# Kernel tuning notes

Measured on AMD Instinct MI355X. Metric: run time of the kernel, lower is better.

The kernel has to match this reference:

```python
import jax, jax.numpy as jnp
import numpy as np

N = 50000      # n_nodes
E = 800000     # n_edges
IN_CH = 128
HID = 128
OUT_CH = 64
N_LAYERS = 4


def _linear_params(key, fan_in, fan_out):
    kw, kb = jax.random.split(key)
    bound = 1.0 / np.sqrt(fan_in)
    W = jax.random.uniform(kw, (fan_out, fan_in), jnp.float32, -bound, bound)
    b = jax.random.uniform(kb, (fan_out,), jnp.float32, -bound, bound)
    return W, b


def setup_inputs() -> dict:
    key = jax.random.key(0)
    ks = jax.random.split(key, 5)
    x = jax.random.normal(ks[0], (N, IN_CH), jnp.float32)
    edge_index = jax.random.randint(ks[1], (2, E), 0, N, dtype=jnp.int64)
    W_in, b_in = _linear_params(ks[2], IN_CH, HID)
    conv_keys = jax.random.split(ks[3], N_LAYERS)
    Wc = jnp.stack([_linear_params(k, HID, HID)[0] for k in conv_keys])
    bc = jnp.stack([_linear_params(k, HID, HID)[1] for k in conv_keys])
    W_out, b_out = _linear_params(ks[4], HID * N_LAYERS, OUT_CH)
    return {"x": x, "edge_index": edge_index, "W_in": W_in, "b_in": b_in,
            "Wc": Wc, "bc": bc, "W_out": W_out, "b_out": b_out}


def reference(x, edge_index, W_in, b_in, Wc, bc, W_out, b_out):
    n = x.shape[0]
    # input projection + relu
    x = jax.nn.relu(x @ W_in.T + b_in)
    src, dst = edge_index[0], edge_index[1]
    loop = jnp.arange(n, dtype=edge_index.dtype)
    src_a = jnp.concatenate([src, loop])   # [E+N]
    dst_a = jnp.concatenate([dst, loop])   # [E+N]
    # symmetric-normalized degree (with self loops)
    deg = jax.ops.segment_sum(jnp.ones(src_a.shape[0], x.dtype), dst_a, num_segments=n)
    norm = (deg[src_a] * deg[dst_a]) ** -0.5
    norm = jnp.where(jnp.isinf(norm), 0.0, norm)  # guard deg==0 (original sets inf->0)
    layer_outputs = []
    for i in range(Wc.shape[0]):
        h = x @ Wc[i].T + bc[i]                     # [N, HID]
        msg = h[src_a] * norm[:, None]              # gather + scale  [E+N, HID]
        out = jax.ops.segment_sum(msg, dst_a, num_segments=n)  # scatter-add
        x = jax.nn.relu(out)
        layer_outputs.append(x)
    h = jnp.concatenate(layer_outputs, axis=-1)     # jk_mode='cat' -> [N, HID*L]
    return h @ W_out.T + b_out
```

## Files before the change

kernel.cpp:

```cpp
#include <hip/hip_runtime.h>
#include <hip/hip_bf16.h>

#ifndef MIN
#define MIN(a,b) ((a)<(b)?(a):(b))
#endif

typedef _Float16 half2_t __attribute__((ext_vector_type(2)));
typedef _Float16 half4_t __attribute__((ext_vector_type(4)));
typedef _Float16 half8_t __attribute__((ext_vector_type(8)));
typedef float floatx4 __attribute__((ext_vector_type(4)));

#define BUCKET_SHIFT 6
#define BUCKET_SIZE 64
#define SCHUNK 2048


template <int KCH, bool A_F16, bool RELU, bool BIAS, bool SCALE, bool F16OUT>
__device__ __forceinline__
void gemm_body64(int rb, int ch, const void* __restrict__ Av, int lda,
                 const _Float16* __restrict__ W, int ldw,
                 const float* __restrict__ bias, const float* __restrict__ dinv,
                 void* __restrict__ Cv, int ldc, int M) {
    __shared__ __align__(16) _Float16 Ws[64][136];

    int tid = threadIdx.x;
    int rowBase = rb * 64;
    int colBase = ch * 64;
    int w = tid >> 6;
    int lane = tid & 63;
    int lrow = lane & 15;
    int quad = lane >> 4;
    int kq = quad * 8;
    int gr = rowBase + w * 16 + lrow;

    floatx4 acc[4];
#pragma unroll
    for (int nt = 0; nt < 4; ++nt) acc[nt] = (floatx4){0.f, 0.f, 0.f, 0.f};

#pragma unroll
    for (int kc = 0; kc < KCH; ++kc) {
#pragma unroll
        for (int i = tid; i < 64 * 16; i += 256) {
            int n = i >> 4, k8 = (i & 15) * 8;
            uint4 v = *(const uint4*)(W + (size_t)(colBase + n) * ldw + kc * 128 + k8);
            *(uint4*)(&Ws[n][k8]) = v;
        }
        __syncthreads();

        half8_t a[4];
        if (gr < M) {
            if (A_F16) {
                const _Float16* A = (const _Float16*)Av;
                const _Float16* ap = A + (size_t)gr * lda + kc * 128 + kq;
#pragma unroll
                for (int ks = 0; ks < 4; ++ks)
                    a[ks] = *(const half8_t*)(ap + ks * 32);
            } else {
                const float* A = (const float*)Av;
                const float* ap = A + (size_t)gr * lda + kc * 128 + kq;
#pragma unroll
                for (int ks = 0; ks < 4; ++ks) {
                    float4 v0 = *(const float4*)(ap + ks * 32);
                    float4 v1 = *(const float4*)(ap + ks * 32 + 4);
                    half8_t h;
                    h[0] = (_Float16)v0.x; h[1] = (_Float16)v0.y;
                    h[2] = (_Float16)v0.z; h[3] = (_Float16)v0.w;
                    h[4] = (_Float16)v1.x; h[5] = (_Float16)v1.y;
                    h[6] = (_Float16)v1.z; h[7] = (_Float16)v1.w;
                    a[ks] = h;
                }
            }
        } else {
#pragma unroll
            for (int ks = 0; ks < 4; ++ks)
                a[ks] = (half8_t){0, 0, 0, 0, 0, 0, 0, 0};
        }

#pragma unroll
        for (int ks = 0; ks < 4; ++ks) {
            int kk = ks * 32 + kq;
#pragma unroll
            for (int nt = 0; nt < 4; ++nt) {
                half8_t b = *(const half8_t*)(&Ws[nt * 16 + lrow][kk]);
                acc[nt] = __builtin_amdgcn_mfma_f32_16x16x32_f16(a[ks], b, acc[nt], 0, 0, 0);
            }
        }
        if (kc != KCH - 1) __syncthreads();
    }

#pragma unroll
    for (int nt = 0; nt < 4; ++nt) {
        int col = colBase + nt * 16 + lrow;
        float bv = BIAS ? bias[col] : 0.0f;
#pragma unroll
        for (int reg = 0; reg < 4; ++reg) {
            int gr2 = rowBase + w * 16 + quad * 4 + reg;
            if (gr2 < M) {
                float v = acc[nt][reg] + bv;
                if (RELU) v = fmaxf(v, 0.0f);
                if (SCALE) v *= dinv[gr2];
                if (F16OUT) {
                    _Float16* C = (_Float16*)Cv;
                    C[(size_t)gr2 * ldc + col] = (_Float16)v;
                } else {
                    float* C = (float*)Cv;
                    C[(size_t)gr2 * ldc + col] = v;
                }
            }
        }
    }
}

template <int KCH, bool A_F16, bool RELU, bool BIAS, bool SCALE, bool F16OUT, bool SPLIT>
__global__ __launch_bounds__(256)
void mfma_gemm64(const void* __restrict__ Av, int lda,
                 const _Float16* __restrict__ W, int ldw,
                 const float* __restrict__ bias, const float* __restrict__ dinv,
                 void* __restrict__ Cv, int ldc, int M) {
    int rb, ch;
    if (SPLIT) { rb = blockIdx.x >> 1; ch = blockIdx.x & 1; }
    else       { rb = blockIdx.x;      ch = 0; }
    gemm_body64<KCH, A_F16, RELU, BIAS, SCALE, F16OUT>(
        rb, ch, Av, lda, W, ldw, bias, dinv, Cv, ldc, M);
}


__global__ __launch_bounds__(256)
void k_hist_cvt(const int* __restrict__ dst, int E, int* __restrict__ bucketCnt, int NB,
                const float* __restrict__ a, _Float16* __restrict__ oa, int na,
                const float* __restrict__ b, _Float16* __restrict__ ob, int nb,
                const float* __restrict__ c, _Float16* __restrict__ oc, int nc,
                _Float16* __restrict__ zrow) {
    __shared__ int h[1024];
    int t = threadIdx.x;
    if (blockIdx.x < 512) {
        for (int i = t; i < 1024; i += 256) h[i] = 0;
        __syncthreads();
        for (int e = blockIdx.x * 256 + t; e < E; e += 512 * 256)
            atomicAdd(&h[dst[e] >> BUCKET_SHIFT], 1);
        __syncthreads();
        for (int i = t; i < NB; i += 256)
            if (h[i]) atomicAdd(&bucketCnt[i], h[i]);
    } else {
        int i = (blockIdx.x - 512) * 256 + t;
        if (i < na) oa[i] = (_Float16)a[i];
        if (i < nb) ob[i] = (_Float16)b[i];
        if (i < nc) oc[i] = (_Float16)c[i];
        if (i < 128) zrow[i] = (_Float16)0.0f;
    }
}

__global__ void bucket_scan(const int* __restrict__ bucketCnt,
                            int* __restrict__ bucketBase, int* __restrict__ bucketCur,
                            int NB, int E) {
    __shared__ int sm[1024];
    int t = threadIdx.x;
    int v = (t < NB) ? bucketCnt[t] : 0;
    sm[t] = v;
    __syncthreads();
    for (int off = 1; off < 1024; off <<= 1) {
        int add = (t >= off) ? sm[t - off] : 0;
        __syncthreads();
        sm[t] += add;
        __syncthreads();
    }
    if (t < NB) {
        bucketBase[t] = sm[t] - v;
        bucketCur[t] = sm[t] - v;
    }
    if (t == 0) bucketBase[NB] = E;
}


__global__ __launch_bounds__(256)
void k_scatter_proj(const int* __restrict__ src, const int* __restrict__ dst, int E,
                    int* __restrict__ bucketCur, unsigned int* __restrict__ rec, int SB,
                    const float* __restrict__ A, const _Float16* __restrict__ W,
                    const float* __restrict__ bias, _Float16* __restrict__ Cout, int M) {
    __shared__ int hist[1024];
    __shared__ int base[1024];
    if (blockIdx.x < SB) {
        int t = threadIdx.x;
        int e0 = blockIdx.x * SCHUNK;
        int e1 = MIN(E, e0 + SCHUNK);
        for (int i = t; i < 1024; i += 256) hist[i] = 0;
        __syncthreads();
        for (int e = e0 + t; e < e1; e += 256)
            atomicAdd(&hist[dst[e] >> BUCKET_SHIFT], 1);
        __syncthreads();
        for (int i = t; i < 1024; i += 256) {
            int c = hist[i];
            base[i] = c ? atomicAdd(&bucketCur[i], c) : 0;
            hist[i] = 0;
        }
        __syncthreads();
        for (int e = e0 + t; e < e1; e += 256) {
            int d = dst[e];
            int bk = d >> BUCKET_SHIFT;
            int pos = base[bk] + atomicAdd(&hist[bk], 1);
            rec[pos] = (unsigned)src[e] | ((unsigned)(d & (BUCKET_SIZE - 1)) << 16);
        }
    } else {
        int b2 = blockIdx.x - SB;
        gemm_body64<1, false, true, true, false, true>(
            b2 >> 1, b2 & 1, A, 128, W, 128, bias, nullptr, Cout, 128, M);
    }
}

__global__ void bucket_build(const unsigned int* __restrict__ rec,
                             const int* __restrict__ bucketBase,
                             int* __restrict__ rowptr, unsigned short* __restrict__ csr_src,
                             float* __restrict__ dinv, int N, int E) {
    __shared__ int lcnt[256];
    __shared__ int sm[256];
    __shared__ int lcur[64];
    int b = blockIdx.x;
    int t = threadIdx.x;
    int beg = bucketBase[b], end = bucketBase[b + 1];
    lcnt[t] = 0;
    __syncthreads();
    for (int i = beg + t; i < end; i += 256)
        atomicAdd(&lcnt[rec[i] >> 16], 1);
    __syncthreads();
    int v = lcnt[t];
    sm[t] = v;
    __syncthreads();
    for (int off = 1; off < 256; off <<= 1) {
        int add = (t >= off) ? sm[t - off] : 0;
        __syncthreads();
        sm[t] += add;
        __syncthreads();
    }
    int excl = sm[t] - v;
    if (t < BUCKET_SIZE) {
        int node = b * BUCKET_SIZE + t;
        if (node < N) {
            rowptr[node] = beg + excl;
            dinv[node] = rsqrtf((float)(v + 1));
        }
        lcur[t] = beg + excl;
    }
    __syncthreads();
    for (int i = beg + t; i < end; i += 256) {
        unsigned int r = rec[i];
        int pos = atomicAdd(&lcur[r >> 16], 1);
        csr_src[pos] = (unsigned short)(r & 0xFFFFu);
    }
    if (b == 0 && t == 0) rowptr[N] = E;
}


__global__ __launch_bounds__(256)
void agg_kernel(const half2_t* __restrict__ Hb, const float* __restrict__ dinv,
                const int* __restrict__ rowptr,
                const unsigned short* __restrict__ csr_src,
                half2_t* __restrict__ X, int N) {
    int node = blockIdx.x * 4 + (threadIdx.x >> 6);
    int t = threadIdx.x & 63;
    if (node >= N) return;
    float di = dinv[node];
    half2_t hu = Hb[(size_t)node * 64 + t];
    float2 acc;
    acc.x = (float)hu.x;
    acc.y = (float)hu.y;
    int beg = rowptr[node];
    int end = rowptr[node + 1];

    for (int base = beg; base < end; base += 64) {
        int idx = base + t;
        int s_lane = (idx < end) ? (int)csr_src[idx] : N;
        int m = end - base;
        if (m > 64) m = 64;
        int mm = (m + 15) & ~15;
        for (int j = 0; j < mm; j += 16) {
            int s[16];
#pragma unroll
            for (int k = 0; k < 16; ++k) s[k] = __shfl(s_lane, j + k);
            half2_t u[16];
#pragma unroll
            for (int k = 0; k < 16; ++k) u[k] = Hb[(size_t)s[k] * 64 + t];
#pragma unroll
            for (int k = 0; k < 16; ++k) {
                acc.x += (float)u[k].x;
                acc.y += (float)u[k].y;
            }
        }
    }
    half2_t o;
    o.x = (_Float16)fmaxf(acc.x * di, 0.0f);
    o.y = (_Float16)fmaxf(acc.y * di, 0.0f);
    X[(size_t)node * 256 + t] = o;
}


extern "C" void kernel_launch(void* const* d_in, const int* in_sizes, int n_in,
                              void* d_out, int out_size, void* d_ws, size_t ws_size,
                              hipStream_t stream) {
    const float* x     = (const float*)d_in[0];
    const int*   ei    = (const int*)d_in[1];
    const float* W_in  = (const float*)d_in[2];
    const float* b_in  = (const float*)d_in[3];
    const float* Wc    = (const float*)d_in[4];
    const float* bc    = (const float*)d_in[5];
    const float* W_out = (const float*)d_in[6];
    const float* b_out = (const float*)d_in[7];
    float* out = (float*)d_out;

    const int HID = 128;
    const int N = in_sizes[0] / HID;
    const int E = in_sizes[1] / 2;
    const int L = 4;
    const int* src = ei;
    const int* dst = ei + E;
    const int NB = (N + BUCKET_SIZE - 1) >> BUCKET_SHIFT;

    char* ws = (char*)d_ws;
    size_t off = 0;
    auto carve = [&](size_t bytes) {
        void* p = ws + off;
        off += (bytes + 255) & ~(size_t)255;
        return p;
    };
    float* dinv        = (float*)carve((size_t)N * 4);
    int*   rowptr      = (int*)carve((size_t)(N + 1) * 4);
    unsigned short* csr_src = (unsigned short*)carve((size_t)E * 2);
    unsigned int* rec  = (unsigned int*)carve((size_t)E * 4);
    int*   bucketCnt   = (int*)carve((size_t)1024 * 4);
    int*   bucketBase  = (int*)carve((size_t)1025 * 4);
    int*   bucketCur   = (int*)carve((size_t)1024 * 4);
    _Float16* bufA     = (_Float16*)carve((size_t)N * HID * 2);
    _Float16* bufH     = (_Float16*)carve((size_t)(N + 1) * HID * 2);
    _Float16* bufXcat  = (_Float16*)carve((size_t)N * 512 * 2);
    _Float16* Wf_in    = (_Float16*)carve((size_t)HID * HID * 2);
    _Float16* Wf_c     = (_Float16*)carve((size_t)L * HID * HID * 2);
    _Float16* Wf_out   = (_Float16*)carve((size_t)64 * 512 * 2);
    (void)ws_size;

    int gemm_blocks = (N + 63) / 64;
    int SB = (E + SCHUNK - 1) / SCHUNK;

    hipMemsetAsync(bucketCnt, 0, (size_t)1024 * 4, stream);
    k_hist_cvt<<<512 + 256, 256, 0, stream>>>(
        dst, E, bucketCnt, NB,
        W_in, Wf_in, HID * HID,
        Wc, Wf_c, L * HID * HID,
        W_out, Wf_out, 64 * 512,
        bufH + (size_t)N * HID);
    bucket_scan<<<1, 1024, 0, stream>>>(bucketCnt, bucketBase, bucketCur, NB, E);
    k_scatter_proj<<<SB + 2 * gemm_blocks, 256, 0, stream>>>(
        src, dst, E, bucketCur, rec, SB,
        x, Wf_in, b_in, bufA, N);
    bucket_build<<<NB, 256, 0, stream>>>(rec, bucketBase, rowptr, csr_src, dinv, N, E);

    for (int l = 0; l < L; ++l) {
        const void* Ain = (l == 0) ? (const void*)bufA
                                   : (const void*)(bufXcat + (size_t)(l - 1) * 128);
        int lda = (l == 0) ? 128 : 512;
        mfma_gemm64<1, true, false, true, true, true, true>
            <<<2 * gemm_blocks, 256, 0, stream>>>(Ain, lda, Wf_c + (size_t)l * HID * HID,
                                                  HID, bc + (size_t)l * HID, dinv,
                                                  bufH, HID, N);
        agg_kernel<<<(N + 3) / 4, 256, 0, stream>>>((const half2_t*)bufH, dinv, rowptr,
                                                    csr_src,
                                                    (half2_t*)bufXcat + (size_t)l * 64, N);
    }

    mfma_gemm64<4, true, false, true, false, false, false>
        <<<gemm_blocks, 256, 0, stream>>>(bufXcat, 512, Wf_out, 512, b_out, nullptr,
                                          out, 64, N);
}
```

Baseline: 310.3 us.

## Split hidden features into 32-column planes for cache-local aggregation passes

The conv GEMM now writes its fp16 output as four column planes of 32 features (each plane holds N+1 rows), not as row-major 128-wide rows. The aggregation kernel runs four passes, one per plane. In each pass a wavefront's 64 lanes gather four neighbors at once, 16 lanes per neighbor and 64 bytes each, and then reduce the partial sums with cross-lane shuffles. The goal is a smaller working set per pass (about 3.2 MB per plane) so random gathers stay in cache. The cost is four times as many agg blocks, shorter 64-byte gather segments, extra shuffle reductions, and scattered GEMM stores.

```diff
diff --git a/kernel.cpp b/kernel.cpp
--- a/kernel.cpp
+++ b/kernel.cpp
@@ -15,7 +15,7 @@
 #define SCHUNK 2048
 
 
-template <int KCH, bool A_F16, bool RELU, bool BIAS, bool SCALE, bool F16OUT>
+template <int KCH, bool A_F16, bool RELU, bool BIAS, bool SCALE, bool F16OUT, bool PLANES>
 __device__ __forceinline__
 void gemm_body64(int rb, int ch, const void* __restrict__ Av, int lda,
                  const _Float16* __restrict__ W, int ldw,
@@ -99,7 +99,11 @@
                 float v = acc[nt][reg] + bv;
                 if (RELU) v = fmaxf(v, 0.0f);
                 if (SCALE) v *= dinv[gr2];
-                if (F16OUT) {
+                if (PLANES) {
+                    _Float16* C = (_Float16*)Cv;
+                    int p = col >> 5, cc = col & 31;
+                    C[((size_t)p * (M + 1) + gr2) * 32 + cc] = (_Float16)v;
+                } else if (F16OUT) {
                     _Float16* C = (_Float16*)Cv;
                     C[(size_t)gr2 * ldc + col] = (_Float16)v;
                 } else {
@@ -111,7 +115,8 @@
     }
 }
 
-template <int KCH, bool A_F16, bool RELU, bool BIAS, bool SCALE, bool F16OUT, bool SPLIT>
+template <int KCH, bool A_F16, bool RELU, bool BIAS, bool SCALE, bool F16OUT, bool PLANES,
+          bool SPLIT>
 __global__ __launch_bounds__(256)
 void mfma_gemm64(const void* __restrict__ Av, int lda,
                  const _Float16* __restrict__ W, int ldw,
@@ -120,7 +125,7 @@
     int rb, ch;
     if (SPLIT) { rb = blockIdx.x >> 1; ch = blockIdx.x & 1; }
     else       { rb = blockIdx.x;      ch = 0; }
-    gemm_body64<KCH, A_F16, RELU, BIAS, SCALE, F16OUT>(
+    gemm_body64<KCH, A_F16, RELU, BIAS, SCALE, F16OUT, PLANES>(
         rb, ch, Av, lda, W, ldw, bias, dinv, Cv, ldc, M);
 }
 
@@ -130,7 +135,7 @@
                 const float* __restrict__ a, _Float16* __restrict__ oa, int na,
                 const float* __restrict__ b, _Float16* __restrict__ ob, int nb,
                 const float* __restrict__ c, _Float16* __restrict__ oc, int nc,
-                _Float16* __restrict__ zrow) {
+                _Float16* __restrict__ planes, int N) {
     __shared__ int h[1024];
     int t = threadIdx.x;
     if (blockIdx.x < 512) {
@@ -146,7 +151,10 @@
         if (i < na) oa[i] = (_Float16)a[i];
         if (i < nb) ob[i] = (_Float16)b[i];
         if (i < nc) oc[i] = (_Float16)c[i];
-        if (i < 128) zrow[i] = (_Float16)0.0f;
+        if (i < 128) {
+            int p = i >> 5, cc = i & 31;
+            planes[((size_t)p * (N + 1) + N) * 32 + cc] = (_Float16)0.0f;
+        }
     }
 }
 
@@ -202,7 +210,7 @@
         }
     } else {
         int b2 = blockIdx.x - SB;
-        gemm_body64<1, false, true, true, false, true>(
+        gemm_body64<1, false, true, true, false, true, false>(
             b2 >> 1, b2 & 1, A, 128, W, 128, bias, nullptr, Cout, 128, M);
     }
 }
@@ -251,20 +259,27 @@
 
 
 __global__ __launch_bounds__(256)
-void agg_kernel(const half2_t* __restrict__ Hb, const float* __restrict__ dinv,
+void agg_kernel(const half2_t* __restrict__ Hp, const float* __restrict__ dinv,
                 const int* __restrict__ rowptr,
                 const unsigned short* __restrict__ csr_src,
-                half2_t* __restrict__ X, int N) {
-    int node = blockIdx.x * 4 + (threadIdx.x >> 6);
+                half2_t* __restrict__ X, int N, int NBLK) {
+    int pass = blockIdx.x / NBLK;
+    int nb = blockIdx.x - pass * NBLK;
+    int node = nb * 4 + (threadIdx.x >> 6);
     int t = threadIdx.x & 63;
     if (node >= N) return;
+    int g = t >> 4;
+    int c = t & 15;
+    const half2_t* P = Hp + (size_t)pass * (N + 1) * 16;
     float di = dinv[node];
-    half2_t hu = Hb[(size_t)node * 64 + t];
+    int beg = rowptr[node];
+    int end = rowptr[node + 1];
+
+    int selfs = (g == 0) ? node : N;
+    half2_t hu = P[(size_t)selfs * 16 + c];
     float2 acc;
     acc.x = (float)hu.x;
     acc.y = (float)hu.y;
-    int beg = rowptr[node];
-    int end = rowptr[node + 1];
 
     for (int base = beg; base < end; base += 64) {
         int idx = base + t;
@@ -273,23 +288,32 @@
         if (m > 64) m = 64;
         int mm = (m + 15) & ~15;
         for (int j = 0; j < mm; j += 16) {
-            int s[16];
-#pragma unroll
-            for (int k = 0; k < 16; ++k) s[k] = __shfl(s_lane, j + k);
-            half2_t u[16];
-#pragma unroll
-            for (int k = 0; k < 16; ++k) u[k] = Hb[(size_t)s[k] * 64 + t];
-#pragma unroll
-            for (int k = 0; k < 16; ++k) {
-                acc.x += (float)u[k].x;
-                acc.y += (float)u[k].y;
-            }
-        }
-    }
-    half2_t o;
-    o.x = (_Float16)fmaxf(acc.x * di, 0.0f);
-    o.y = (_Float16)fmaxf(acc.y * di, 0.0f);
-    X[(size_t)node * 256 + t] = o;
+            int s0 = __shfl(s_lane, j + g);
+            int s1 = __shfl(s_lane, j + 4 + g);
+            int s2 = __shfl(s_lane, j + 8 + g);
+            int s3 = __shfl(s_lane, j + 12 + g);
+            half2_t u0 = P[(size_t)s0 * 16 + c];
+            half2_t u1 = P[(size_t)s1 * 16 + c];
+            half2_t u2 = P[(size_t)s2 * 16 + c];
+            half2_t u3 = P[(size_t)s3 * 16 + c];
+            acc.x += (float)u0.x; acc.y += (float)u0.y;
+            acc.x += (float)u1.x; acc.y += (float)u1.y;
+            acc.x += (float)u2.x; acc.y += (float)u2.y;
+            acc.x += (float)u3.x; acc.y += (float)u3.y;
+        }
+    }
+
+    acc.x += __shfl_xor(acc.x, 16);
+    acc.x += __shfl_xor(acc.x, 32);
+    acc.y += __shfl_xor(acc.y, 16);
+    acc.y += __shfl_xor(acc.y, 32);
+
+    if (g == 0) {
+        half2_t o;
+        o.x = (_Float16)fmaxf(acc.x * di, 0.0f);
+        o.y = (_Float16)fmaxf(acc.y * di, 0.0f);
+        X[(size_t)node * 256 + pass * 16 + c] = o;
+    }
 }
 
 
@@ -329,7 +353,7 @@
     int*   bucketBase  = (int*)carve((size_t)1025 * 4);
     int*   bucketCur   = (int*)carve((size_t)1024 * 4);
     _Float16* bufA     = (_Float16*)carve((size_t)N * HID * 2);
-    _Float16* bufH     = (_Float16*)carve((size_t)(N + 1) * HID * 2);
+    _Float16* bufHpl   = (_Float16*)carve((size_t)4 * (N + 1) * 32 * 2);
     _Float16* bufXcat  = (_Float16*)carve((size_t)N * 512 * 2);
     _Float16* Wf_in    = (_Float16*)carve((size_t)HID * HID * 2);
     _Float16* Wf_c     = (_Float16*)carve((size_t)L * HID * HID * 2);
@@ -338,6 +362,7 @@
 
     int gemm_blocks = (N + 63) / 64;
     int SB = (E + SCHUNK - 1) / SCHUNK;
+    int NBLK = (N + 3) / 4;
 
     hipMemsetAsync(bucketCnt, 0, (size_t)1024 * 4, stream);
     k_hist_cvt<<<512 + 256, 256, 0, stream>>>(
@@ -345,7 +370,7 @@
         W_in, Wf_in, HID * HID,
         Wc, Wf_c, L * HID * HID,
         W_out, Wf_out, 64 * 512,
-        bufH + (size_t)N * HID);
+        bufHpl, N);
     bucket_scan<<<1, 1024, 0, stream>>>(bucketCnt, bucketBase, bucketCur, NB, E);
     k_scatter_proj<<<SB + 2 * gemm_blocks, 256, 0, stream>>>(
         src, dst, E, bucketCur, rec, SB,
@@ -356,16 +381,17 @@
         const void* Ain = (l == 0) ? (const void*)bufA
                                    : (const void*)(bufXcat + (size_t)(l - 1) * 128);
         int lda = (l == 0) ? 128 : 512;
-        mfma_gemm64<1, true, false, true, true, true, true>
+        mfma_gemm64<1, true, false, true, true, true, true, true>
             <<<2 * gemm_blocks, 256, 0, stream>>>(Ain, lda, Wf_c + (size_t)l * HID * HID,
                                                   HID, bc + (size_t)l * HID, dinv,
-                                                  bufH, HID, N);
-        agg_kernel<<<(N + 3) / 4, 256, 0, stream>>>((const half2_t*)bufH, dinv, rowptr,
-                                                    csr_src,
-                                                    (half2_t*)bufXcat + (size_t)l * 64, N);
-    }
-
-    mfma_gemm64<4, true, false, true, false, false, false>
+                                                  bufHpl, 0, N);
+        agg_kernel<<<4 * NBLK, 256, 0, stream>>>((const half2_t*)bufHpl, dinv, rowptr,
+                                                 csr_src,
+                                                 (half2_t*)bufXcat + (size_t)l * 64,
+                                                 N, NBLK);
+    }
+
+    mfma_gemm64<4, true, false, true, false, false, false, false>
         <<<gemm_blocks, 256, 0, stream>>>(bufXcat, 512, Wf_out, 512, b_out, nullptr,
                                           out, 64, N);
 }
```

New measurement: 429.2 us. 1.38x slower.

## Split node range in halves to overlap aggregation with next-layer GEMM

Applied to the files above, without the earlier changes.

Each layer's aggregation now runs in two halves. The second half is launched together with the next layer's GEMM over the first half's rows, which is ready by then, and the final output GEMM is overlapped the same way. The intent is to hide GEMM cost behind the memory-bound gather and to fill the GPU better at kernel tails. H is double-buffered so the next GEMM can write while the gather reads. The weight-tile load is also moved after the A-fragment loads so their latency overlaps. This adds more launches and mixed-role blocks, which could imbalance the GPU.

```diff
diff --git a/kernel.cpp b/kernel.cpp
--- a/kernel.cpp
+++ b/kernel.cpp
@@ -39,14 +39,6 @@
 
 #pragma unroll
     for (int kc = 0; kc < KCH; ++kc) {
-#pragma unroll
-        for (int i = tid; i < 64 * 16; i += 256) {
-            int n = i >> 4, k8 = (i & 15) * 8;
-            uint4 v = *(const uint4*)(W + (size_t)(colBase + n) * ldw + kc * 128 + k8);
-            *(uint4*)(&Ws[n][k8]) = v;
-        }
-        __syncthreads();
-
         half8_t a[4];
         if (gr < M) {
             if (A_F16) {
@@ -75,6 +67,14 @@
             for (int ks = 0; ks < 4; ++ks)
                 a[ks] = (half8_t){0, 0, 0, 0, 0, 0, 0, 0};
         }
+
+#pragma unroll
+        for (int i = tid; i < 64 * 16; i += 256) {
+            int n = i >> 4, k8 = (i & 15) * 8;
+            uint4 v = *(const uint4*)(W + (size_t)(colBase + n) * ldw + kc * 128 + k8);
+            *(uint4*)(&Ws[n][k8]) = v;
+        }
+        __syncthreads();
 
 #pragma unroll
         for (int ks = 0; ks < 4; ++ks) {
@@ -116,12 +116,98 @@
 void mfma_gemm64(const void* __restrict__ Av, int lda,
                  const _Float16* __restrict__ W, int ldw,
                  const float* __restrict__ bias, const float* __restrict__ dinv,
-                 void* __restrict__ Cv, int ldc, int M) {
+                 void* __restrict__ Cv, int ldc, int M, int rbOff) {
     int rb, ch;
-    if (SPLIT) { rb = blockIdx.x >> 1; ch = blockIdx.x & 1; }
-    else       { rb = blockIdx.x;      ch = 0; }
+    if (SPLIT) { rb = (blockIdx.x >> 1) + rbOff; ch = blockIdx.x & 1; }
+    else       { rb = blockIdx.x + rbOff;        ch = 0; }
     gemm_body64<KCH, A_F16, RELU, BIAS, SCALE, F16OUT>(
         rb, ch, Av, lda, W, ldw, bias, dinv, Cv, ldc, M);
+}
+
+
+__device__ __forceinline__
+void agg_body(int nodeBlk, int lo, const half2_t* __restrict__ Hb,
+              const float* __restrict__ dinv, const int* __restrict__ rowptr,
+              const unsigned short* __restrict__ csr_src,
+              half2_t* __restrict__ X, int N) {
+    int node = lo + nodeBlk * 4 + (threadIdx.x >> 6);
+    int t = threadIdx.x & 63;
+    if (node >= N) return;
+    float di = dinv[node];
+    half2_t hu = Hb[(size_t)node * 64 + t];
+    float2 acc;
+    acc.x = (float)hu.x;
+    acc.y = (float)hu.y;
+    int beg = rowptr[node];
+    int end = rowptr[node + 1];
+
+    for (int base = beg; base < end; base += 64) {
+        int idx = base + t;
+        int s_lane = (idx < end) ? (int)csr_src[idx] : N;
+        int m = end - base;
+        if (m > 64) m = 64;
+        int mm = (m + 15) & ~15;
+        for (int j = 0; j < mm; j += 16) {
+            int s[16];
+#pragma unroll
+            for (int k = 0; k < 16; ++k) s[k] = __shfl(s_lane, j + k);
+            half2_t u[16];
+#pragma unroll
+            for (int k = 0; k < 16; ++k) u[k] = Hb[(size_t)s[k] * 64 + t];
+#pragma unroll
+            for (int k = 0; k < 16; ++k) {
+                acc.x += (float)u[k].x;
+                acc.y += (float)u[k].y;
+            }
+        }
+    }
+    half2_t o;
+    o.x = (_Float16)fmaxf(acc.x * di, 0.0f);
+    o.y = (_Float16)fmaxf(acc.y * di, 0.0f);
+    X[(size_t)node * 256 + t] = o;
+}
+
+__global__ __launch_bounds__(256)
+void agg_kernel(const half2_t* __restrict__ Hb, const float* __restrict__ dinv,
+                const int* __restrict__ rowptr,
+                const unsigned short* __restrict__ csr_src,
+                half2_t* __restrict__ X, int N, int lo) {
+    agg_body(blockIdx.x, lo, Hb, dinv, rowptr, csr_src, X, N);
+}
+
+
+__global__ __launch_bounds__(256)
+void k_agg_conv(const half2_t* __restrict__ Hin, const float* __restrict__ dinv,
+                const int* __restrict__ rowptr,
+                const unsigned short* __restrict__ csr_src,
+                half2_t* __restrict__ Xslab, int N, int lo, int aggN,
+                const _Float16* __restrict__ Ain, int lda,
+                const _Float16* __restrict__ W, const float* __restrict__ bias,
+                _Float16* __restrict__ Hout, int rbOff) {
+    if ((int)blockIdx.x < aggN) {
+        agg_body(blockIdx.x, lo, Hin, dinv, rowptr, csr_src, Xslab, N);
+    } else {
+        int b2 = blockIdx.x - aggN;
+        gemm_body64<1, true, false, true, true, true>(
+            (b2 >> 1) + rbOff, b2 & 1, Ain, lda, W, 128, bias, dinv, Hout, 128, N);
+    }
+}
+
+__global__ __launch_bounds__(256)
+void k_agg_out(const half2_t* __restrict__ Hin, const float* __restrict__ dinv,
+               const int* __restrict__ rowptr,
+               const unsigned short* __restrict__ csr_src,
+               half2_t* __restrict__ Xslab, int N, int lo, int aggN,
+               const _Float16* __restrict__ Xcat,
+               const _Float16* __restrict__ W, const float* __restrict__ bias,
+               float* __restrict__ out, int rbOff) {
+    if ((int)blockIdx.x < aggN) {
+        agg_body(blockIdx.x, lo, Hin, dinv, rowptr, csr_src, Xslab, N);
+    } else {
+        int b2 = blockIdx.x - aggN;
+        gemm_body64<4, true, false, true, false, false>(
+            b2 + rbOff, 0, Xcat, 512, W, 512, bias, nullptr, out, 64, N);
+    }
 }
 
 
@@ -130,7 +216,7 @@
                 const float* __restrict__ a, _Float16* __restrict__ oa, int na,
                 const float* __restrict__ b, _Float16* __restrict__ ob, int nb,
                 const float* __restrict__ c, _Float16* __restrict__ oc, int nc,
-                _Float16* __restrict__ zrow) {
+                _Float16* __restrict__ zrow1, _Float16* __restrict__ zrow2) {
     __shared__ int h[1024];
     int t = threadIdx.x;
     if (blockIdx.x < 512) {
@@ -146,7 +232,7 @@
         if (i < na) oa[i] = (_Float16)a[i];
         if (i < nb) ob[i] = (_Float16)b[i];
         if (i < nc) oc[i] = (_Float16)c[i];
-        if (i < 128) zrow[i] = (_Float16)0.0f;
+        if (i < 128) { zrow1[i] = (_Float16)0.0f; zrow2[i] = (_Float16)0.0f; }
     }
 }
 
@@ -250,49 +336,6 @@
 }
 
 
-__global__ __launch_bounds__(256)
-void agg_kernel(const half2_t* __restrict__ Hb, const float* __restrict__ dinv,
-                const int* __restrict__ rowptr,
-                const unsigned short* __restrict__ csr_src,
-                half2_t* __restrict__ X, int N) {
-    int node = blockIdx.x * 4 + (threadIdx.x >> 6);
-    int t = threadIdx.x & 63;
-    if (node >= N) return;
-    float di = dinv[node];
-    half2_t hu = Hb[(size_t)node * 64 + t];
-    float2 acc;
-    acc.x = (float)hu.x;
-    acc.y = (float)hu.y;
-    int beg = rowptr[node];
-    int end = rowptr[node + 1];
-
-    for (int base = beg; base < end; base += 64) {
-        int idx = base + t;
-        int s_lane = (idx < end) ? (int)csr_src[idx] : N;
-        int m = end - base;
-        if (m > 64) m = 64;
-        int mm = (m + 15) & ~15;
-        for (int j = 0; j < mm; j += 16) {
-            int s[16];
-#pragma unroll
-            for (int k = 0; k < 16; ++k) s[k] = __shfl(s_lane, j + k);
-            half2_t u[16];
-#pragma unroll
-            for (int k = 0; k < 16; ++k) u[k] = Hb[(size_t)s[k] * 64 + t];
-#pragma unroll
-            for (int k = 0; k < 16; ++k) {
-                acc.x += (float)u[k].x;
-                acc.y += (float)u[k].y;
-            }
-        }
-    }
-    half2_t o;
-    o.x = (_Float16)fmaxf(acc.x * di, 0.0f);
-    o.y = (_Float16)fmaxf(acc.y * di, 0.0f);
-    X[(size_t)node * 256 + t] = o;
-}
-
-
 extern "C" void kernel_launch(void* const* d_in, const int* in_sizes, int n_in,
                               void* d_out, int out_size, void* d_ws, size_t ws_size,
                               hipStream_t stream) {
@@ -329,7 +372,8 @@
     int*   bucketBase  = (int*)carve((size_t)1025 * 4);
     int*   bucketCur   = (int*)carve((size_t)1024 * 4);
     _Float16* bufA     = (_Float16*)carve((size_t)N * HID * 2);
-    _Float16* bufH     = (_Float16*)carve((size_t)(N + 1) * HID * 2);
+    _Float16* bufHa    = (_Float16*)carve((size_t)(N + 1) * HID * 2);
+    _Float16* bufHb    = (_Float16*)carve((size_t)(N + 1) * HID * 2);
     _Float16* bufXcat  = (_Float16*)carve((size_t)N * 512 * 2);
     _Float16* Wf_in    = (_Float16*)carve((size_t)HID * HID * 2);
     _Float16* Wf_c     = (_Float16*)carve((size_t)L * HID * HID * 2);
@@ -338,6 +382,14 @@
 
     int gemm_blocks = (N + 63) / 64;
     int SB = (E + SCHUNK - 1) / SCHUNK;
+    int HALF_RB = (gemm_blocks + 1) / 2;
+    int RB1 = gemm_blocks - HALF_RB;
+    int HALF = HALF_RB * 64;
+    int hi0 = MIN(HALF, N);
+    int AGG0 = (hi0 + 3) / 4;
+    int AGG1 = (N - hi0 + 3) / 4;
+
+    _Float16* Hbuf[2] = {bufHa, bufHb};
 
     hipMemsetAsync(bucketCnt, 0, (size_t)1024 * 4, stream);
     k_hist_cvt<<<512 + 256, 256, 0, stream>>>(
@@ -345,27 +397,45 @@
         W_in, Wf_in, HID * HID,
         Wc, Wf_c, L * HID * HID,
         W_out, Wf_out, 64 * 512,
-        bufH + (size_t)N * HID);
+        bufHa + (size_t)N * HID, bufHb + (size_t)N * HID);
     bucket_scan<<<1, 1024, 0, stream>>>(bucketCnt, bucketBase, bucketCur, NB, E);
     k_scatter_proj<<<SB + 2 * gemm_blocks, 256, 0, stream>>>(
         src, dst, E, bucketCur, rec, SB,
         x, Wf_in, b_in, bufA, N);
     bucket_build<<<NB, 256, 0, stream>>>(rec, bucketBase, rowptr, csr_src, dinv, N, E);
 
-    for (int l = 0; l < L; ++l) {
-        const void* Ain = (l == 0) ? (const void*)bufA
-                                   : (const void*)(bufXcat + (size_t)(l - 1) * 128);
-        int lda = (l == 0) ? 128 : 512;
+    mfma_gemm64<1, true, false, true, true, true, true>
+        <<<2 * gemm_blocks, 256, 0, stream>>>(bufA, 128, Wf_c, 128, bc, dinv,
+                                              bufHa, 128, N, 0);
+
+    for (int l = 0; l < 3; ++l) {
+        const half2_t* Hin = (const half2_t*)Hbuf[l & 1];
+        _Float16* Hout = Hbuf[(l + 1) & 1];
+        half2_t* Xslab = (half2_t*)bufXcat + (size_t)l * 64;
+        const _Float16* Xin = bufXcat + (size_t)l * 128;
+
+        agg_kernel<<<AGG0, 256, 0, stream>>>(Hin, dinv, rowptr, csr_src, Xslab, N, 0);
+        k_agg_conv<<<AGG1 + 2 * HALF_RB, 256, 0, stream>>>(
+            Hin, dinv, rowptr, csr_src, Xslab, N, hi0, AGG1,
+            Xin, 512, Wf_c + (size_t)(l + 1) * HID * HID, bc + (size_t)(l + 1) * HID,
+            Hout, 0);
         mfma_gemm64<1, true, false, true, true, true, true>
-            <<<2 * gemm_blocks, 256, 0, stream>>>(Ain, lda, Wf_c + (size_t)l * HID * HID,
-                                                  HID, bc + (size_t)l * HID, dinv,
-                                                  bufH, HID, N);
-        agg_kernel<<<(N + 3) / 4, 256, 0, stream>>>((const half2_t*)bufH, dinv, rowptr,
-                                                    csr_src,
-                                                    (half2_t*)bufXcat + (size_t)l * 64, N);
-    }
-
-    mfma_gemm64<4, true, false, true, false, false, false>
-        <<<gemm_blocks, 256, 0, stream>>>(bufXcat, 512, Wf_out, 512, b_out, nullptr,
-                                          out, 64, N);
-}
+            <<<2 * RB1, 256, 0, stream>>>(Xin, 512,
+                                          Wf_c + (size_t)(l + 1) * HID * HID, 128,
+                                          bc + (size_t)(l + 1) * HID, dinv,
+                                          Hout, 128, N, HALF_RB);
+    }
+
+    {
+        const half2_t* Hin = (const half2_t*)Hbuf[3 & 1];
+        half2_t* Xslab = (half2_t*)bufXcat + (size_t)3 * 64;
+
+        agg_kernel<<<AGG0, 256, 0, stream>>>(Hin, dinv, rowptr, csr_src, Xslab, N, 0);
+        k_agg_out<<<AGG1 + HALF_RB, 256, 0, stream>>>(
+            Hin, dinv, rowptr, csr_src, Xslab, N, hi0, AGG1,
+            bufXcat, Wf_out, b_out, out, 0);
+        mfma_gemm64<4, true, false, true, false, false, false>
+            <<<RB1, 256, 0, stream>>>(bufXcat, 512, Wf_out, 512, b_out, nullptr,
+                                      out, 64, N, HALF_RB);
+    }
+}
```

Result: slower. 348.2 us (+12.2%).

## Overlap first three K-chunks of output GEMM with last-layer aggregation

Applied to the files above, without the earlier changes.

Splits the final output projection into two parts. The first 384 input columns come from layers 0-2, so their GEMM runs in the same launch as the layer-3 aggregation, using extra blocks. A small accumulate GEMM then adds the last 128 columns into the fp32 output. The goal is to hide most of the output GEMM behind the memory-bound aggregation, at the cost of an extra read-modify-write of the output and one more launch.

```diff
diff --git a/kernel.cpp b/kernel.cpp
--- a/kernel.cpp
+++ b/kernel.cpp
@@ -15,7 +15,7 @@
 #define SCHUNK 2048
 
 
-template <int KCH, bool A_F16, bool RELU, bool BIAS, bool SCALE, bool F16OUT>
+template <int KCH, bool A_F16, bool RELU, bool BIAS, bool SCALE, bool F16OUT, bool ACCUM>
 __device__ __forceinline__
 void gemm_body64(int rb, int ch, const void* __restrict__ Av, int lda,
                  const _Float16* __restrict__ W, int ldw,
@@ -104,6 +104,7 @@
                     C[(size_t)gr2 * ldc + col] = (_Float16)v;
                 } else {
                     float* C = (float*)Cv;
+                    if (ACCUM) v += C[(size_t)gr2 * ldc + col];
                     C[(size_t)gr2 * ldc + col] = v;
                 }
             }
@@ -111,7 +112,8 @@
     }
 }
 
-template <int KCH, bool A_F16, bool RELU, bool BIAS, bool SCALE, bool F16OUT, bool SPLIT>
+template <int KCH, bool A_F16, bool RELU, bool BIAS, bool SCALE, bool F16OUT, bool ACCUM,
+          bool SPLIT>
 __global__ __launch_bounds__(256)
 void mfma_gemm64(const void* __restrict__ Av, int lda,
                  const _Float16* __restrict__ W, int ldw,
@@ -120,8 +122,77 @@
     int rb, ch;
     if (SPLIT) { rb = blockIdx.x >> 1; ch = blockIdx.x & 1; }
     else       { rb = blockIdx.x;      ch = 0; }
-    gemm_body64<KCH, A_F16, RELU, BIAS, SCALE, F16OUT>(
+    gemm_body64<KCH, A_F16, RELU, BIAS, SCALE, F16OUT, ACCUM>(
         rb, ch, Av, lda, W, ldw, bias, dinv, Cv, ldc, M);
+}
+
+
+__device__ __forceinline__
+void agg_body(int nodeBlk, const half2_t* __restrict__ Hb,
+              const float* __restrict__ dinv, const int* __restrict__ rowptr,
+              const unsigned short* __restrict__ csr_src,
+              half2_t* __restrict__ X, int N) {
+    int node = nodeBlk * 4 + (threadIdx.x >> 6);
+    int t = threadIdx.x & 63;
+    if (node >= N) return;
+    float di = dinv[node];
+    half2_t hu = Hb[(size_t)node * 64 + t];
+    float2 acc;
+    acc.x = (float)hu.x;
+    acc.y = (float)hu.y;
+    int beg = rowptr[node];
+    int end = rowptr[node + 1];
+
+    for (int base = beg; base < end; base += 64) {
+        int idx = base + t;
+        int s_lane = (idx < end) ? (int)csr_src[idx] : N;
+        int m = end - base;
+        if (m > 64) m = 64;
+        int mm = (m + 15) & ~15;
+        for (int j = 0; j < mm; j += 16) {
+            int s[16];
+#pragma unroll
+            for (int k = 0; k < 16; ++k) s[k] = __shfl(s_lane, j + k);
+            half2_t u[16];
+#pragma unroll
+            for (int k = 0; k < 16; ++k) u[k] = Hb[(size_t)s[k] * 64 + t];
+#pragma unroll
+            for (int k = 0; k < 16; ++k) {
+                acc.x += (float)u[k].x;
+                acc.y += (float)u[k].y;
+            }
+        }
+    }
+    half2_t o;
+    o.x = (_Float16)fmaxf(acc.x * di, 0.0f);
+    o.y = (_Float16)fmaxf(acc.y * di, 0.0f);
+    X[(size_t)node * 256 + t] = o;
+}
+
+__global__ __launch_bounds__(256)
+void agg_kernel(const half2_t* __restrict__ Hb, const float* __restrict__ dinv,
+                const int* __restrict__ rowptr,
+                const unsigned short* __restrict__ csr_src,
+                half2_t* __restrict__ X, int N) {
+    agg_body(blockIdx.x, Hb, dinv, rowptr, csr_src, X, N);
+}
+
+
+__global__ __launch_bounds__(256)
+void k_agg_out(const half2_t* __restrict__ Hin, const float* __restrict__ dinv,
+               const int* __restrict__ rowptr,
+               const unsigned short* __restrict__ csr_src,
+               half2_t* __restrict__ Xslab, int N, int aggN,
+               const _Float16* __restrict__ Xcat,
+               const _Float16* __restrict__ W, const float* __restrict__ bias,
+               float* __restrict__ out) {
+    if ((int)blockIdx.x < aggN) {
+        agg_body(blockIdx.x, Hin, dinv, rowptr, csr_src, Xslab, N);
+    } else {
+        int b2 = blockIdx.x - aggN;
+        gemm_body64<3, true, false, true, false, false, false>(
+            b2, 0, Xcat, 512, W, 512, bias, nullptr, out, 64, N);
+    }
 }
 
 
@@ -202,7 +273,7 @@
         }
     } else {
         int b2 = blockIdx.x - SB;
-        gemm_body64<1, false, true, true, false, true>(
+        gemm_body64<1, false, true, true, false, true, false>(
             b2 >> 1, b2 & 1, A, 128, W, 128, bias, nullptr, Cout, 128, M);
     }
 }
@@ -247,49 +318,6 @@
         csr_src[pos] = (unsigned short)(r & 0xFFFFu);
     }
     if (b == 0 && t == 0) rowptr[N] = E;
-}
-
-
-__global__ __launch_bounds__(256)
-void agg_kernel(const half2_t* __restrict__ Hb, const float* __restrict__ dinv,
-                const int* __restrict__ rowptr,
-                const unsigned short* __restrict__ csr_src,
-                half2_t* __restrict__ X, int N) {
-    int node = blockIdx.x * 4 + (threadIdx.x >> 6);
-    int t = threadIdx.x & 63;
-    if (node >= N) return;
-    float di = dinv[node];
-    half2_t hu = Hb[(size_t)node * 64 + t];
-    float2 acc;
-    acc.x = (float)hu.x;
-    acc.y = (float)hu.y;
-    int beg = rowptr[node];
-    int end = rowptr[node + 1];
-
-    for (int base = beg; base < end; base += 64) {
-        int idx = base + t;
-        int s_lane = (idx < end) ? (int)csr_src[idx] : N;
-        int m = end - base;
-        if (m > 64) m = 64;
-        int mm = (m + 15) & ~15;
-        for (int j = 0; j < mm; j += 16) {
-            int s[16];
-#pragma unroll
-            for (int k = 0; k < 16; ++k) s[k] = __shfl(s_lane, j + k);
-            half2_t u[16];
-#pragma unroll
-            for (int k = 0; k < 16; ++k) u[k] = Hb[(size_t)s[k] * 64 + t];
-#pragma unroll
-            for (int k = 0; k < 16; ++k) {
-                acc.x += (float)u[k].x;
-                acc.y += (float)u[k].y;
-            }
-        }
-    }
-    half2_t o;
-    o.x = (_Float16)fmaxf(acc.x * di, 0.0f);
-    o.y = (_Float16)fmaxf(acc.y * di, 0.0f);
-    X[(size_t)node * 256 + t] = o;
 }
 
 
@@ -338,6 +366,7 @@
 
     int gemm_blocks = (N + 63) / 64;
     int SB = (E + SCHUNK - 1) / SCHUNK;
+    int AGGN = (N + 3) / 4;
 
     hipMemsetAsync(bucketCnt, 0, (size_t)1024 * 4, stream);
     k_hist_cvt<<<512 + 256, 256, 0, stream>>>(
@@ -356,16 +385,23 @@
         const void* Ain = (l == 0) ? (const void*)bufA
                                    : (const void*)(bufXcat + (size_t)(l - 1) * 128);
         int lda = (l == 0) ? 128 : 512;
-        mfma_gemm64<1, true, false, true, true, true, true>
+        mfma_gemm64<1, true, false, true, true, true, false, true>
             <<<2 * gemm_blocks, 256, 0, stream>>>(Ain, lda, Wf_c + (size_t)l * HID * HID,
                                                   HID, bc + (size_t)l * HID, dinv,
                                                   bufH, HID, N);
-        agg_kernel<<<(N + 3) / 4, 256, 0, stream>>>((const half2_t*)bufH, dinv, rowptr,
-                                                    csr_src,
-                                                    (half2_t*)bufXcat + (size_t)l * 64, N);
-    }
-
-    mfma_gemm64<4, true, false, true, false, false, false>
-        <<<gemm_blocks, 256, 0, stream>>>(bufXcat, 512, Wf_out, 512, b_out, nullptr,
-                                          out, 64, N);
-}
+        if (l < 3) {
+            agg_kernel<<<AGGN, 256, 0, stream>>>((const half2_t*)bufH, dinv, rowptr,
+                                                 csr_src,
+                                                 (half2_t*)bufXcat + (size_t)l * 64, N);
+        } else {
+            k_agg_out<<<AGGN + gemm_blocks, 256, 0, stream>>>(
+                (const half2_t*)bufH, dinv, rowptr, csr_src,
+                (half2_t*)bufXcat + (size_t)3 * 64, N, AGGN,
+                bufXcat, Wf_out, b_out, out);
+        }
+    }
+
+    mfma_gemm64<1, true, false, false, false, false, true, false>
+        <<<gemm_blocks, 256, 0, stream>>>(bufXcat + 384, 512, Wf_out + 384, 512,
+                                          nullptr, nullptr, out, 64, N);
+}
```

Measured after the change: 320.2 us. 1.03x slower.
